# Performance work log

Measured on AMD Instinct MI355X. Metric: run time of the kernel, lower is better.

## Reference

```python
import jax, jax.numpy as jnp
import numpy as np

D_MODEL = 4096
RANK = 16
BATCH = 4
SEQ = 4096


def setup_inputs() -> dict:
    key = jax.random.key(0)
    k_x, k_w, k_b, k_a, k_bb = jax.random.split(key, 5)
    x = jax.random.normal(k_x, (BATCH, SEQ, D_MODEL), dtype=jnp.float32)
    W = jax.random.normal(k_w, (D_MODEL, D_MODEL), dtype=jnp.float32) * 0.02
    bias = jax.random.normal(k_b, (D_MODEL,), dtype=jnp.float32) * 0.02
    A = jax.random.normal(k_a, (D_MODEL, RANK), dtype=jnp.float32) * 0.01
    B = jax.random.normal(k_bb, (RANK, D_MODEL), dtype=jnp.float32) * 0.01
    return {"x": x, "W": W, "bias": bias, "A": A, "B": B}


def reference(x, W, bias, A, B):
    # Faithful to the torch module: delta_W = A @ B; linear(x, W + delta_W, bias)
    # i.e. out = x @ (W + A @ B)^T + bias, with W: [d_out, d_in], x: [b, s, d_in].
    delta_W = A @ B                                   # [d_out, d_in]
    out = jnp.einsum("bsi,oi->bso", x, W + delta_W) + bias
    return out
```

## Files before the change

kernel.cpp:

```cpp
#include <hip/hip_runtime.h>
#include <stdint.h>


#define MDIM 16384
#define NDIM 4096
#define KDIM 4096
#define RANK 16
#define NT   (KDIM / 64)

typedef __bf16  bf16x8 __attribute__((ext_vector_type(8)));
typedef float   f32x4  __attribute__((ext_vector_type(4)));
typedef unsigned short u16x8 __attribute__((ext_vector_type(8)));

__device__ __forceinline__ unsigned short f2bf(float f) {
  union { float f; uint32_t u; } v; v.f = f;
  uint32_t r = v.u + 0x7FFFu + ((v.u >> 16) & 1u);
  return (unsigned short)(r >> 16);
}

__device__ __forceinline__ void gl16(const void* g, void* l) {
  __builtin_amdgcn_global_load_lds(
      (__attribute__((address_space(1))) void*)(g),
      (__attribute__((address_space(3))) void*)(l),
      16, 0, 0);
}

__global__ void prep_w(const float* __restrict__ W, const float* __restrict__ A,
                       const float* __restrict__ Bm, unsigned short* __restrict__ Wp) {
  const int i = blockIdx.x * 256 + threadIdx.x;
  const int o = blockIdx.y;
  float acc = W[(size_t)o * NDIM + i];
#pragma unroll
  for (int r = 0; r < RANK; ++r)
    acc += A[o * RANK + r] * Bm[(size_t)r * NDIM + i];
  Wp[(size_t)o * NDIM + i] = f2bf(acc);
}

__global__ void cast_x(const float* __restrict__ x, unsigned short* __restrict__ xb) {
  const size_t i = ((size_t)blockIdx.x * 256 + threadIdx.x) * 8;
  float4 a = *(const float4*)(x + i);
  float4 b = *(const float4*)(x + i + 4);
  u16x8 o;
  o[0] = f2bf(a.x); o[1] = f2bf(a.y); o[2] = f2bf(a.z); o[3] = f2bf(a.w);
  o[4] = f2bf(b.x); o[5] = f2bf(b.y); o[6] = f2bf(b.z); o[7] = f2bf(b.w);
  *(u16x8*)(xb + i) = o;
}

#define BARRIER  __builtin_amdgcn_s_barrier()
#define WAITLGKM asm volatile("s_waitcnt lgkmcnt(0)" ::: "memory")
#define WAITVM2  asm volatile("s_waitcnt vmcnt(2)" ::: "memory")
#define WAITVM0  asm volatile("s_waitcnt vmcnt(0)" ::: "memory")
#define SCHEDB   __builtin_amdgcn_sched_barrier(0)

#define STAGE(buf, h4, kt) do {                                                   \
    const int kc_ = ((kt) < NT ? (kt) : NT - 1);                                  \
    const unsigned short* g_ = (((h4) & 2) ? bgb : agb)                           \
        + (size_t)(((h4) & 1) * 128) * KDIM + kc_ * 64;                           \
    unsigned short* d_ = (((h4) & 2) ? &sB[(buf)][0] : &sA[(buf)][0])             \
        + ((h4) & 1) * 8192 + t * 8;                                              \
    gl16(g_, d_);                                                                 \
    gl16(g_ + (size_t)64 * KDIM, d_ + 4096);                                      \
  } while (0)

#define LDA(buf, mh) do {                                                         \
    _Pragma("unroll") for (int mi = 0; mi < 4; ++mi)                              \
    _Pragma("unroll") for (int kk = 0; kk < 2; ++kk)                              \
      a[mi][kk] = *(const bf16x8*)(saw + (buf)*16384 + ((mh)*64 + mi*16)*64       \
                                   + ((kk*32 + koff) ^ xorE));                    \
  } while (0)

#define LDB(buf, nh, bb) do {                                                     \
    _Pragma("unroll") for (int ni = 0; ni < 2; ++ni)                              \
    _Pragma("unroll") for (int kk = 0; kk < 2; ++kk)                              \
      bb[ni][kk] = *(const bf16x8*)(sbw + (buf)*16384 + ((nh)*32 + ni*16)*64      \
                                    + ((kk*32 + koff) ^ xorE));                   \
  } while (0)

#define MM(mh, nh, bb) do {                                                       \
    __builtin_amdgcn_s_setprio(1);                                                \
    _Pragma("unroll") for (int mi = 0; mi < 4; ++mi)                              \
    _Pragma("unroll") for (int ni = 0; ni < 2; ++ni)                              \
    _Pragma("unroll") for (int kk = 0; kk < 2; ++kk)                              \
      acc[(mh)*4+mi][(nh)*2+ni] = __builtin_amdgcn_mfma_f32_16x16x32_bf16(        \
          a[mi][kk], bb[ni][kk], acc[(mh)*4+mi][(nh)*2+ni], 0, 0, 0);             \
    __builtin_amdgcn_s_setprio(0);                                                \
  } while (0)

__global__ __launch_bounds__(512, 2) void gemm256(
    const unsigned short* __restrict__ Xb,
    const unsigned short* __restrict__ Wp,
    const float* __restrict__ bias,
    float* __restrict__ out) {
  __shared__ __align__(16) unsigned short sA[2][256 * 64];
  __shared__ __align__(16) unsigned short sB[2][256 * 64];

  const int t  = threadIdx.x;
  const int l  = t & 63;
  const int w  = t >> 6;
  const int wm = w >> 2;
  const int wn = w & 3;

  const int bid = blockIdx.x;
  const int swz = (bid & 7) * (1024 / 8) + (bid >> 3);
  const int bm  = (swz >> 4) * 256;
  const int bn  = (swz & 15) * 256;

  const int sr  = t >> 3;
  const int ske = (((t & 7) * 16) ^ ((sr & 7) << 4)) >> 1;
  const unsigned short* agb = Xb + (size_t)(bm + sr) * KDIM + ske;
  const unsigned short* bgb = Wp + (size_t)(bn + sr) * KDIM + ske;

  const int lr   = l & 15;
  const int koff = (l >> 4) * 8;
  const int xorE = (lr & 7) << 3;
  const unsigned short* saw = &sA[0][0] + (wm * 128 + lr) * 64;
  const unsigned short* sbw = &sB[0][0] + (wn * 64 + lr) * 64;

  bf16x8 a[4][2], b0[2][2], b1[2][2];
  f32x4 acc[8][4];
#pragma unroll
  for (int i = 0; i < 8; ++i)
#pragma unroll
    for (int j = 0; j < 4; ++j)
      acc[i][j] = f32x4{0.f, 0.f, 0.f, 0.f};

  STAGE(0, 0, 0); STAGE(0, 1, 0); STAGE(0, 2, 0); STAGE(0, 3, 0);
  STAGE(1, 0, 1);
  WAITVM2;
  BARRIER;

  for (int it = 0; it < NT / 2; ++it) {
    const int E = it * 2;
    LDA(0, 0); LDB(0, 0, b0);
    STAGE(1, 1, E + 1);
    BARRIER; WAITLGKM; SCHEDB;
    MM(0, 0, b0);
    BARRIER;
    LDB(0, 1, b1);
    STAGE(1, 2, E + 1);
    BARRIER; WAITLGKM; SCHEDB;
    MM(0, 1, b1);
    BARRIER;
    LDA(0, 1);
    STAGE(1, 3, E + 1);
    BARRIER; WAITLGKM; SCHEDB;
    MM(1, 1, b1);
    BARRIER;
    STAGE(0, 0, E + 2);
    BARRIER;
    MM(1, 0, b0);
    WAITVM2;
    BARRIER;
    LDA(1, 0); LDB(1, 0, b0);
    STAGE(0, 1, E + 2);
    BARRIER; WAITLGKM; SCHEDB;
    MM(0, 0, b0);
    BARRIER;
    LDB(1, 1, b1);
    STAGE(0, 2, E + 2);
    BARRIER; WAITLGKM; SCHEDB;
    MM(0, 1, b1);
    BARRIER;
    LDA(1, 1);
    STAGE(0, 3, E + 2);
    BARRIER; WAITLGKM; SCHEDB;
    MM(1, 1, b1);
    BARRIER;
    STAGE(1, 0, E + 3);
    BARRIER;
    MM(1, 0, b0);
    WAITVM2;
    BARRIER;
  }

  WAITVM0;

#pragma unroll
  for (int mf = 0; mf < 8; ++mf) {
#pragma unroll
    for (int nf = 0; nf < 4; ++nf) {
      const int row = bm + wm * 128 + mf * 16 + (l >> 4) * 4;
      const int col = bn + wn * 64 + nf * 16 + lr;
      const float bv = bias[col];
#pragma unroll
      for (int r = 0; r < 4; ++r)
        out[(size_t)(row + r) * NDIM + col] = acc[mf][nf][r] + bv;
    }
  }
}

extern "C" void kernel_launch(void* const* d_in, const int* in_sizes, int n_in,
                              void* d_out, int out_size, void* d_ws, size_t ws_size,
                              hipStream_t stream) {
  const float* x    = (const float*)d_in[0];
  const float* W    = (const float*)d_in[1];
  const float* bias = (const float*)d_in[2];
  const float* A    = (const float*)d_in[3];
  const float* B    = (const float*)d_in[4];
  float* out        = (float*)d_out;

  unsigned short* Wp = (unsigned short*)d_ws;
  unsigned short* Xb = (unsigned short*)d_ws + (size_t)NDIM * KDIM;

  prep_w<<<dim3(NDIM / 256, NDIM), 256, 0, stream>>>(W, A, B, Wp);
  cast_x<<<dim3((size_t)MDIM * KDIM / (256 * 8)), 256, 0, stream>>>(x, Xb);
  gemm256<<<dim3((MDIM / 256) * (NDIM / 256)), 512, 0, stream>>>(Xb, Wp, bias, out);
}
```

Measured before the change: 629.6 us.

## Interleave A/B tile staging and deepen prefetch with finer vmcnt waits

Reorganizes how each 256x64 A and B tile is split into staged halves, so each wave's M and N sub-tiles are interleaved (rows h*64 and h*64+128 for A, h*32 strided for B). LDS fragment addressing and global row mapping change to match. Stages for the next buffer are issued earlier in the loop, and vmcnt waits are relaxed to allow more outstanding global loads, with the aim of hiding memory latency better. This risks ordering hazards if a buffer's loads have not finished when it is read, and it adds more in-flight loads.

```diff
diff --git a/kernel.cpp b/kernel.cpp
--- a/kernel.cpp
+++ b/kernel.cpp
@@ -48,42 +48,49 @@
 
 #define BARRIER  __builtin_amdgcn_s_barrier()
 #define WAITLGKM asm volatile("s_waitcnt lgkmcnt(0)" ::: "memory")
-#define WAITVM2  asm volatile("s_waitcnt vmcnt(2)" ::: "memory")
+#define VMCNT8   asm volatile("s_waitcnt vmcnt(8)" ::: "memory")
+#define VMCNT6   asm volatile("s_waitcnt vmcnt(6)" ::: "memory")
 #define WAITVM0  asm volatile("s_waitcnt vmcnt(0)" ::: "memory")
 #define SCHEDB   __builtin_amdgcn_sched_barrier(0)
 
-#define STAGE(buf, h4, kt) do {                                                   \
-    const int kc_ = ((kt) < NT ? (kt) : NT - 1);                                  \
-    const unsigned short* g_ = (((h4) & 2) ? bgb : agb)                           \
-        + (size_t)(((h4) & 1) * 128) * KDIM + kc_ * 64;                           \
-    unsigned short* d_ = (((h4) & 2) ? &sB[(buf)][0] : &sA[(buf)][0])             \
-        + ((h4) & 1) * 8192 + t * 8;                                              \
-    gl16(g_, d_);                                                                 \
-    gl16(g_ + (size_t)64 * KDIM, d_ + 4096);                                      \
-  } while (0)
-
-#define LDA(buf, mh) do {                                                         \
-    _Pragma("unroll") for (int mi = 0; mi < 4; ++mi)                              \
-    _Pragma("unroll") for (int kk = 0; kk < 2; ++kk)                              \
-      a[mi][kk] = *(const bf16x8*)(saw + (buf)*16384 + ((mh)*64 + mi*16)*64       \
-                                   + ((kk*32 + koff) ^ xorE));                    \
-  } while (0)
-
-#define LDB(buf, nh, bb) do {                                                     \
-    _Pragma("unroll") for (int ni = 0; ni < 2; ++ni)                              \
-    _Pragma("unroll") for (int kk = 0; kk < 2; ++kk)                              \
-      bb[ni][kk] = *(const bf16x8*)(sbw + (buf)*16384 + ((nh)*32 + ni*16)*64      \
-                                    + ((kk*32 + koff) ^ xorE));                   \
-  } while (0)
-
-#define MM(mh, nh, bb) do {                                                       \
-    __builtin_amdgcn_s_setprio(1);                                                \
-    _Pragma("unroll") for (int mi = 0; mi < 4; ++mi)                              \
-    _Pragma("unroll") for (int ni = 0; ni < 2; ++ni)                              \
-    _Pragma("unroll") for (int kk = 0; kk < 2; ++kk)                              \
-      acc[(mh)*4+mi][(nh)*2+ni] = __builtin_amdgcn_mfma_f32_16x16x32_bf16(        \
-          a[mi][kk], bb[ni][kk], acc[(mh)*4+mi][(nh)*2+ni], 0, 0, 0);             \
-    __builtin_amdgcn_s_setprio(0);                                                \
+#define STAGE_A(buf, h, kt) do {                                              \
+    const int kc_ = ((kt) < NT ? (kt) : NT - 1);                              \
+    const unsigned short* g_ = agb + (size_t)((h) * 64) * KDIM + kc_ * 64;    \
+    unsigned short* d_ = &sA[(buf)][0] + (h) * 8192 + t * 8;                  \
+    gl16(g_, d_);                                                             \
+    gl16(g_ + (size_t)128 * KDIM, d_ + 4096);                                 \
+  } while (0)
+
+#define STAGE_B(buf, h, kt) do {                                              \
+    const int kc_ = ((kt) < NT ? (kt) : NT - 1);                              \
+    const unsigned short* g_ = bgb + (size_t)((h) * 32) * KDIM + kc_ * 64;    \
+    unsigned short* d_ = &sB[(buf)][0] + (h) * 8192 + t * 8;                  \
+    gl16(g_, d_);                                                             \
+    gl16(g_ + (size_t)128 * KDIM, d_ + 4096);                                 \
+  } while (0)
+
+#define LDA(buf, mh) do {                                                     \
+    _Pragma("unroll") for (int mi = 0; mi < 4; ++mi)                          \
+    _Pragma("unroll") for (int kk = 0; kk < 2; ++kk)                          \
+      a[mi][kk] = *(const bf16x8*)(saw + (buf)*16384 + ((mh)*128 + mi*16)*64  \
+                                   + ((kk*32 + koff) ^ xorE));                \
+  } while (0)
+
+#define LDB(buf, nh, bb) do {                                                 \
+    _Pragma("unroll") for (int ni = 0; ni < 2; ++ni)                          \
+    _Pragma("unroll") for (int kk = 0; kk < 2; ++kk)                          \
+      bb[ni][kk] = *(const bf16x8*)(sbw + (buf)*16384 + ((nh)*128 + ni*16)*64 \
+                                    + ((kk*32 + koff) ^ xorE));               \
+  } while (0)
+
+#define MM(mh, nh, bb) do {                                                   \
+    __builtin_amdgcn_s_setprio(1);                                            \
+    _Pragma("unroll") for (int mi = 0; mi < 4; ++mi)                          \
+    _Pragma("unroll") for (int ni = 0; ni < 2; ++ni)                          \
+    _Pragma("unroll") for (int kk = 0; kk < 2; ++kk)                          \
+      acc[(mh)*4+mi][(nh)*2+ni] = __builtin_amdgcn_mfma_f32_16x16x32_bf16(    \
+          a[mi][kk], bb[ni][kk], acc[(mh)*4+mi][(nh)*2+ni], 0, 0, 0);         \
+    __builtin_amdgcn_s_setprio(0);                                            \
   } while (0)
 
 __global__ __launch_bounds__(512, 2) void gemm256(
@@ -108,13 +115,13 @@
   const int sr  = t >> 3;
   const int ske = (((t & 7) * 16) ^ ((sr & 7) << 4)) >> 1;
   const unsigned short* agb = Xb + (size_t)(bm + sr) * KDIM + ske;
-  const unsigned short* bgb = Wp + (size_t)(bn + sr) * KDIM + ske;
+  const unsigned short* bgb = Wp + (size_t)(bn + (sr >> 5) * 64 + (sr & 31)) * KDIM + ske;
 
   const int lr   = l & 15;
   const int koff = (l >> 4) * 8;
   const int xorE = (lr & 7) << 3;
-  const unsigned short* saw = &sA[0][0] + (wm * 128 + lr) * 64;
-  const unsigned short* sbw = &sB[0][0] + (wn * 64 + lr) * 64;
+  const unsigned short* saw = &sA[0][0] + (wm * 64 + lr) * 64;
+  const unsigned short* sbw = &sB[0][0] + (wn * 32 + lr) * 64;
 
   bf16x8 a[4][2], b0[2][2], b1[2][2];
   f32x4 acc[8][4];
@@ -124,52 +131,54 @@
     for (int j = 0; j < 4; ++j)
       acc[i][j] = f32x4{0.f, 0.f, 0.f, 0.f};
 
-  STAGE(0, 0, 0); STAGE(0, 1, 0); STAGE(0, 2, 0); STAGE(0, 3, 0);
-  STAGE(1, 0, 1);
-  WAITVM2;
+  STAGE_A(0, 0, 0); STAGE_B(0, 0, 0); STAGE_A(0, 1, 0); STAGE_B(0, 1, 0);
+  STAGE_A(1, 0, 1); STAGE_B(1, 0, 1); STAGE_B(1, 1, 1);
+  VMCNT6;
   BARRIER;
 
   for (int it = 0; it < NT / 2; ++it) {
     const int E = it * 2;
     LDA(0, 0); LDB(0, 0, b0);
-    STAGE(1, 1, E + 1);
+    STAGE_A(1, 1, E + 1);
     BARRIER; WAITLGKM; SCHEDB;
     MM(0, 0, b0);
     BARRIER;
     LDB(0, 1, b1);
-    STAGE(1, 2, E + 1);
+    STAGE_A(0, 0, E + 2);
     BARRIER; WAITLGKM; SCHEDB;
     MM(0, 1, b1);
+    VMCNT8;
     BARRIER;
     LDA(0, 1);
-    STAGE(1, 3, E + 1);
+    STAGE_B(0, 0, E + 2);
     BARRIER; WAITLGKM; SCHEDB;
     MM(1, 1, b1);
     BARRIER;
-    STAGE(0, 0, E + 2);
+    STAGE_B(0, 1, E + 2);
     BARRIER;
     MM(1, 0, b0);
-    WAITVM2;
+    VMCNT8;
     BARRIER;
     LDA(1, 0); LDB(1, 0, b0);
-    STAGE(0, 1, E + 2);
+    STAGE_A(0, 1, E + 2);
     BARRIER; WAITLGKM; SCHEDB;
     MM(0, 0, b0);
     BARRIER;
     LDB(1, 1, b1);
-    STAGE(0, 2, E + 2);
+    STAGE_A(1, 0, E + 3);
     BARRIER; WAITLGKM; SCHEDB;
     MM(0, 1, b1);
+    VMCNT8;
     BARRIER;
     LDA(1, 1);
-    STAGE(0, 3, E + 2);
+    STAGE_B(1, 0, E + 3);
     BARRIER; WAITLGKM; SCHEDB;
     MM(1, 1, b1);
     BARRIER;
-    STAGE(1, 0, E + 3);
+    STAGE_B(1, 1, E + 3);
     BARRIER;
     MM(1, 0, b0);
-    WAITVM2;
+    VMCNT8;
     BARRIER;
   }
 
```

Result: no change. 636.4 us (+1.1%).
